# Performance work log

Measured on AMD Instinct MI355X. Metric: run time of the kernel, lower is better.

The kernel has to match this reference:

```python
import jax, jax.numpy as jnp
import numpy as np

B, CIN, H, W = 8, 64, 128, 128
COUT, K = 64, 3
STRIDE, PAD, DIL, G = 1, 1, 1, 1
T = K * K
HO = (H + 2 * PAD - (DIL * (K - 1) + 1)) // STRIDE + 1
WO = (W + 2 * PAD - (DIL * (K - 1) + 1)) // STRIDE + 1


def setup_inputs() -> dict:
    key = jax.random.key(0)
    ks = jax.random.split(key, 5)
    x = jax.random.normal(ks[0], (B, CIN, H, W), jnp.float32)
    offset = jax.random.normal(ks[1], (B, 2 * G * T, HO, WO), jnp.float32)
    mask = jax.random.uniform(ks[2], (B, G * T, HO, WO), jnp.float32)
    weight = jax.random.normal(ks[3], (COUT, CIN, K, K), jnp.float32) * (1.0 / np.sqrt(CIN * T))
    bias = jnp.zeros((COUT,), jnp.float32)
    return {"x": x, "offset": offset, "mask": mask, "weight": weight, "bias": bias}


def _gather(img_f, idx):
    # img_f: [Cg, H*W], idx: [T, Ho, Wo] -> [Cg, T, Ho, Wo]
    return img_f[:, idx]


def _dcn(x, offset, mask, weight, bias):
    Bn, Cin, Hh, Ww = x.shape
    Cout = weight.shape[0]
    Cg = Cin // G
    # offset channels laid out as [G, T, (dy, dx)] per DCNv2 convention
    off = offset.reshape(Bn, G, T, 2, HO, WO)
    dy, dx = off[:, :, :, 0], off[:, :, :, 1]  # [B, G, T, Ho, Wo]
    ky, kx = jnp.meshgrid(jnp.arange(K), jnp.arange(K), indexing="ij")
    ky = (ky.reshape(T) * DIL).astype(jnp.float32)
    kx = (kx.reshape(T) * DIL).astype(jnp.float32)
    base_y = (jnp.arange(HO) * STRIDE - PAD).astype(jnp.float32)
    base_x = (jnp.arange(WO) * STRIDE - PAD).astype(jnp.float32)
    # absolute sampling coordinates per (batch, def-group, tap, out-row, out-col)
    py = dy + base_y[None, None, None, :, None] + ky[None, None, :, None, None]
    px = dx + base_x[None, None, None, None, :] + kx[None, None, :, None, None]
    y0 = jnp.floor(py)
    x0 = jnp.floor(px)
    imgf = x.reshape(Bn, G, Cg, Hh * Ww)
    gather = jax.vmap(jax.vmap(_gather))  # over B and G
    sampled = jnp.zeros((Bn, G, Cg, T, HO, WO), x.dtype)
    # bilinear interpolation with zero padding outside the image
    for oy, ox in ((y0, x0), (y0, x0 + 1.0), (y0 + 1.0, x0), (y0 + 1.0, x0 + 1.0)):
        wgt = (1.0 - jnp.abs(py - oy)) * (1.0 - jnp.abs(px - ox))
        valid = (oy >= 0) & (oy < Hh) & (ox >= 0) & (ox < Ww)
        yi = jnp.clip(oy, 0, Hh - 1).astype(jnp.int32)
        xi = jnp.clip(ox, 0, Ww - 1).astype(jnp.int32)
        vals = gather(imgf, yi * Ww + xi)  # [B, G, Cg, T, Ho, Wo]
        sampled = sampled + vals * (wgt * valid)[:, :, None]
    # modulation mask, then accumulate taps into output channels
    m = mask.reshape(Bn, G, T, HO, WO)
    sampled = sampled * m[:, :, None]
    wr = weight.reshape(Cout, G, Cg, T)
    out = jnp.einsum("bgctij,ogct->boij", sampled, wr) + bias[None, :, None, None]
    return out


def reference(x, offset, mask, weight, bias):
    return _dcn(x, offset, mask, weight, bias)
```

## Files before the change

### kernel.cpp

```cpp
#include <hip/hip_runtime.h>
#include <stdint.h>

#define Bn   8
#define CIN  64
#define Hh   128
#define Wh   128
#define COUT 64
#define Tt   9
#define HO   128
#define WO   128
#define HW   (HO * WO)

#define RH     15
#define RWC    23
#define RREC   (RH * RWC)
#define RSTR   144
#define HALO_Y 3
#define HALO_X 3

typedef _Float16 h16;
typedef __attribute__((ext_vector_type(2)))  _Float16 h2;
typedef __attribute__((ext_vector_type(8)))  _Float16 h8;
typedef __attribute__((ext_vector_type(16))) float    f16v;

__device__ h16 g_xT[(size_t)Bn * Hh * Wh * CIN];
__device__ h16 g_wh[Tt * 4 * 2 * 64 * 8];

__global__ __launch_bounds__(256) void prep(const float* __restrict__ x,
                                            const float* __restrict__ w) {
    if (blockIdx.x >= Bn * Hh) {
        int tid = (blockIdx.x - Bn * Hh) * 256 + threadIdx.x;
        int t   = tid >> 12;
        int rem = tid & 4095;
        int ks  = rem >> 10;
        int mt  = (rem >> 9) & 1;
        int ln  = (rem >> 3) & 63;
        int j   = rem & 7;
        int o   = mt * 32 + (ln & 31);
        int c   = ks * 16 + ((ln >> 5) << 3) + j;
        g_wh[tid] = (h16)w[(size_t)(o * 64 + c) * 9 + t];
        return;
    }
    int b = blockIdx.x >> 7;
    int y = blockIdx.x & 127;
    __shared__ uint32_t tile[64][65];

    const float* src = x + ((size_t)b * CIN) * (Hh * Wh) + (size_t)y * Wh;
    int t    = threadIdx.x;
    int xp   = t & 63;
    int csub = t >> 6;
    #pragma unroll
    for (int cc = 0; cc < 64; cc += 4) {
        int c = cc + csub;
        float2 v = *(const float2*)(src + (size_t)c * (Hh * Wh) + xp * 2);
        uint32_t h0 = (uint32_t)__builtin_bit_cast(uint16_t, (h16)v.x);
        uint32_t h1 = (uint32_t)__builtin_bit_cast(uint16_t, (h16)v.y);
        tile[c][xp] = h0 | (h1 << 16);
    }
    __syncthreads();

    uint32_t* dst = (uint32_t*)(g_xT + (((size_t)b * Hh + y) * Wh) * CIN);
    int d  = t & 31;
    int xo = t >> 5;
    #pragma unroll
    for (int it = 0; it < 16; ++it) {
        int xg = it * 8 + xo;
        uint32_t lo = tile[2 * d][xg >> 1];
        uint32_t hi = tile[2 * d + 1][xg >> 1];
        int sh = (xg & 1) * 16;
        uint32_t l0 = (lo >> sh) & 0xffffu;
        uint32_t h1 = (hi >> sh) & 0xffffu;
        dst[xg * 32 + d] = l0 | (h1 << 16);
    }
}

__global__ __launch_bounds__(256, 3) void dcn_main(
        const float* __restrict__ offset, const float* __restrict__ mask,
        const float* __restrict__ bias, float* __restrict__ out) {
    __shared__ __align__(16) uint8_t sreg[RREC * RSTR];

    int blk  = blockIdx.x;
    int b    = blk & 7;
    int s    = blk >> 3;
    int ty   = s >> 3, tx = s & 7;
    int i0   = ty * 8, j0 = tx * 16;
    int lane = threadIdx.x & 63;
    int wave = threadIdx.x >> 6;
    int n    = lane & 31;
    int g    = lane >> 5;

    const h16* xb = g_xT + (size_t)b * (Hh * Wh * CIN);

    int i = i0 + 2 * wave + (n >> 4);
    int j = j0 + (n & 15);
    int p = (i << 7) + j;

    const float* offB = offset + (size_t)b * (2 * Tt * HW);
    const float* mskB = mask   + (size_t)b * (Tt * HW);
    float dyv[Tt], dxv[Tt], mmv[Tt];
    #pragma unroll
    for (int t = 0; t < Tt; ++t) {
        dyv[t] = offB[(2 * t) * HW + p];
        dxv[t] = offB[(2 * t + 1) * HW + p];
        mmv[t] = mskB[t * HW + p];
    }

    {
        const int base_y = i0 - HALO_Y, base_x = j0 - HALO_X;
        #pragma unroll
        for (int it = 0; it < 11; ++it) {
            int idx  = it * 256 + threadIdx.x;
            int rec  = idx >> 3;
            int quad = idx & 7;
            if (rec < RREC) {
                int ry = rec / RWC, rx = rec - ry * RWC;
                int gy = min(max(base_y + ry, 0), Hh - 1);
                int gx = min(max(base_x + rx, 0), Wh - 1);
                uint4 v = *(const uint4*)(xb + ((gy << 7) + gx) * 64 + quad * 8);
                *(uint4*)(sreg + rec * RSTR + quad * 16) = v;
            }
        }
    }
    __syncthreads();

    f16v acc[2] = {};

    #pragma unroll
    for (int t = 0; t < Tt; ++t) {
        const int ky = t / 3, kx = t % 3;
        float py = dyv[t] + (float)(i + ky - 1);
        float px = dxv[t] + (float)(j + kx - 1);
        float fy = floorf(py), fx = floorf(px);
        int   y0 = (int)fy,    x0 = (int)fx;
        float ly = py - fy,    lx = px - fx;
        float hy = 1.f - ly,   hx = 1.f - lx;

        bool vy0 = (y0 >= 0) && (y0 < Hh);
        bool vy1 = (y0 >= -1) && (y0 < Hh - 1);
        bool vx0 = (x0 >= 0) && (x0 < Wh);
        bool vx1 = (x0 >= -1) && (x0 < Wh - 1);
        float m = mmv[t];
        float w00 = (vy0 && vx0) ? hy * hx * m : 0.f;
        float w01 = (vy0 && vx1) ? hy * lx * m : 0.f;
        float w10 = (vy1 && vx0) ? ly * hx * m : 0.f;
        float w11 = (vy1 && vx1) ? ly * lx * m : 0.f;

        int ry = y0 - i0 + HALO_Y;
        int rx = x0 - j0 + HALO_X;
        bool intile = (ry >= 0) & (ry <= RH - 2) & (rx >= 0) & (rx <= RWC - 2);
        int ryc = min(max(ry, 0), RH - 2), rxc = min(max(rx, 0), RWC - 2);
        int pl00 = ryc * RWC + rxc;
        const uint8_t* cbase = sreg + pl00 * RSTR + g * 16;

        bool fb_any = __any(!intile);
        const h16 *f00 = nullptr, *f01 = nullptr, *f10 = nullptr, *f11 = nullptr;
        if (fb_any) {
            int y0c = min(max(y0, 0), Hh - 1), y1c = min(max(y0 + 1, 0), Hh - 1);
            int x0c = min(max(x0, 0), Wh - 1), x1c = min(max(x0 + 1, 0), Wh - 1);
            const h16* r0 = xb + (size_t)(y0c * Wh) * CIN;
            const h16* r1 = xb + (size_t)(y1c * Wh) * CIN;
            f00 = r0 + x0c * CIN + g * 8;
            f01 = r0 + x1c * CIN + g * 8;
            f10 = r1 + x0c * CIN + g * 8;
            f11 = r1 + x1c * CIN + g * 8;
        }

        h2 W00 = {(h16)w00, (h16)w00};
        h2 W01 = {(h16)w01, (h16)w01};
        h2 W10 = {(h16)w10, (h16)w10};
        h2 W11 = {(h16)w11, (h16)w11};

        const h16* wt = g_wh + t * 4096;
        union U4 { uint4 v; h2 h[4]; };
        #pragma unroll
        for (int ks = 0; ks < 4; ++ks) {
            U4 c00, c01, c10, c11;
            const uint8_t* cb = cbase + ks * 32;
            c00.v = *(const uint4*)(cb);
            c01.v = *(const uint4*)(cb + RSTR);
            c10.v = *(const uint4*)(cb + RWC * RSTR);
            c11.v = *(const uint4*)(cb + (RWC + 1) * RSTR);
            if (fb_any) {
                if (!intile) {
                    c00.v = *(const uint4*)(f00 + ks * 16);
                    c01.v = *(const uint4*)(f01 + ks * 16);
                    c10.v = *(const uint4*)(f10 + ks * 16);
                    c11.v = *(const uint4*)(f11 + ks * 16);
                }
            }
            union { h2 r[4]; h8 v; } pk;
            #pragma unroll
            for (int e = 0; e < 4; ++e) {
                h2 r = c00.h[e] * W00;
                r = c01.h[e] * W01 + r;
                r = c10.h[e] * W10 + r;
                r = c11.h[e] * W11 + r;
                pk.r[e] = r;
            }
            #pragma unroll
            for (int mt = 0; mt < 2; ++mt) {
                h8 a = *(const h8*)(wt + (ks * 2 + mt) * 512 + lane * 8);
                acc[mt] = __builtin_amdgcn_mfma_f32_32x32x16_f16(
                    a, pk.v, acc[mt], 0, 0, 0);
            }
        }
    }

    #pragma unroll
    for (int mt = 0; mt < 2; ++mt) {
        #pragma unroll
        for (int r = 0; r < 16; ++r) {
            int o = mt * 32 + (r & 3) + 8 * (r >> 2) + 4 * g;
            out[(size_t)(b * COUT + o) * HW + p] = acc[mt][r] + bias[o];
        }
    }
}

extern "C" void kernel_launch(void* const* d_in, const int* in_sizes, int n_in,
                              void* d_out, int out_size, void* d_ws, size_t ws_size,
                              hipStream_t stream) {
    const float* x      = (const float*)d_in[0];
    const float* offset = (const float*)d_in[1];
    const float* mask   = (const float*)d_in[2];
    const float* weight = (const float*)d_in[3];
    const float* bias   = (const float*)d_in[4];
    (void)d_ws; (void)ws_size;

    prep<<<Bn * Hh + 144, 256, 0, stream>>>(x, weight);
    dcn_main<<<Bn * 128, 256, 0, stream>>>(offset, mask, bias, (float*)d_out);
}
```

Baseline: 127.9 us.

## Drop LDS halo staging and gather bilinear corners directly from global memory

Removes the shared-memory staging of each block's 15x23 channel-last halo region, along with the fallback path for samples outside the tile. Every bilinear corner is now gathered directly from the global fp16 NHWC copy, relying on L1/L2 caching. Without LDS, occupancy rises and launch bounds go from 3 to 4 blocks per CU. The cost is more global/L2 gather traffic and latency, since nearby taps that previously hit LDS now go through the cache hierarchy.

```diff
diff --git a/kernel.cpp b/kernel.cpp
--- a/kernel.cpp
+++ b/kernel.cpp
@@ -10,13 +10,6 @@
 #define HO   128
 #define WO   128
 #define HW   (HO * WO)
-
-#define RH     15
-#define RWC    23
-#define RREC   (RH * RWC)
-#define RSTR   144
-#define HALO_Y 3
-#define HALO_X 3
 
 typedef _Float16 h16;
 typedef __attribute__((ext_vector_type(2)))  _Float16 h2;
@@ -74,11 +67,9 @@
     }
 }
 
-__global__ __launch_bounds__(256, 3) void dcn_main(
+__global__ __launch_bounds__(256, 4) void dcn_main(
         const float* __restrict__ offset, const float* __restrict__ mask,
         const float* __restrict__ bias, float* __restrict__ out) {
-    __shared__ __align__(16) uint8_t sreg[RREC * RSTR];
-
     int blk  = blockIdx.x;
     int b    = blk & 7;
     int s    = blk >> 3;
@@ -105,24 +96,6 @@
         mmv[t] = mskB[t * HW + p];
     }
 
-    {
-        const int base_y = i0 - HALO_Y, base_x = j0 - HALO_X;
-        #pragma unroll
-        for (int it = 0; it < 11; ++it) {
-            int idx  = it * 256 + threadIdx.x;
-            int rec  = idx >> 3;
-            int quad = idx & 7;
-            if (rec < RREC) {
-                int ry = rec / RWC, rx = rec - ry * RWC;
-                int gy = min(max(base_y + ry, 0), Hh - 1);
-                int gx = min(max(base_x + rx, 0), Wh - 1);
-                uint4 v = *(const uint4*)(xb + ((gy << 7) + gx) * 64 + quad * 8);
-                *(uint4*)(sreg + rec * RSTR + quad * 16) = v;
-            }
-        }
-    }
-    __syncthreads();
-
     f16v acc[2] = {};
 
     #pragma unroll
@@ -145,25 +118,12 @@
         float w10 = (vy1 && vx0) ? ly * hx * m : 0.f;
         float w11 = (vy1 && vx1) ? ly * lx * m : 0.f;
 
-        int ry = y0 - i0 + HALO_Y;
-        int rx = x0 - j0 + HALO_X;
-        bool intile = (ry >= 0) & (ry <= RH - 2) & (rx >= 0) & (rx <= RWC - 2);
-        int ryc = min(max(ry, 0), RH - 2), rxc = min(max(rx, 0), RWC - 2);
-        int pl00 = ryc * RWC + rxc;
-        const uint8_t* cbase = sreg + pl00 * RSTR + g * 16;
-
-        bool fb_any = __any(!intile);
-        const h16 *f00 = nullptr, *f01 = nullptr, *f10 = nullptr, *f11 = nullptr;
-        if (fb_any) {
-            int y0c = min(max(y0, 0), Hh - 1), y1c = min(max(y0 + 1, 0), Hh - 1);
-            int x0c = min(max(x0, 0), Wh - 1), x1c = min(max(x0 + 1, 0), Wh - 1);
-            const h16* r0 = xb + (size_t)(y0c * Wh) * CIN;
-            const h16* r1 = xb + (size_t)(y1c * Wh) * CIN;
-            f00 = r0 + x0c * CIN + g * 8;
-            f01 = r0 + x1c * CIN + g * 8;
-            f10 = r1 + x0c * CIN + g * 8;
-            f11 = r1 + x1c * CIN + g * 8;
-        }
+        int y0c = min(max(y0, 0), Hh - 1), y1c = min(max(y0 + 1, 0), Hh - 1);
+        int x0c = min(max(x0, 0), Wh - 1), x1c = min(max(x0 + 1, 0), Wh - 1);
+        const h16* p00 = xb + (((y0c << 7) | x0c) << 6) + g * 8;
+        const h16* p01 = xb + (((y0c << 7) | x1c) << 6) + g * 8;
+        const h16* p10 = xb + (((y1c << 7) | x0c) << 6) + g * 8;
+        const h16* p11 = xb + (((y1c << 7) | x1c) << 6) + g * 8;
 
         h2 W00 = {(h16)w00, (h16)w00};
         h2 W01 = {(h16)w01, (h16)w01};
@@ -175,19 +135,10 @@
         #pragma unroll
         for (int ks = 0; ks < 4; ++ks) {
             U4 c00, c01, c10, c11;
-            const uint8_t* cb = cbase + ks * 32;
-            c00.v = *(const uint4*)(cb);
-            c01.v = *(const uint4*)(cb + RSTR);
-            c10.v = *(const uint4*)(cb + RWC * RSTR);
-            c11.v = *(const uint4*)(cb + (RWC + 1) * RSTR);
-            if (fb_any) {
-                if (!intile) {
-                    c00.v = *(const uint4*)(f00 + ks * 16);
-                    c01.v = *(const uint4*)(f01 + ks * 16);
-                    c10.v = *(const uint4*)(f10 + ks * 16);
-                    c11.v = *(const uint4*)(f11 + ks * 16);
-                }
-            }
+            c00.v = *(const uint4*)(p00 + ks * 16);
+            c01.v = *(const uint4*)(p01 + ks * 16);
+            c10.v = *(const uint4*)(p10 + ks * 16);
+            c11.v = *(const uint4*)(p11 + ks * 16);
             union { h2 r[4]; h8 v; } pk;
             #pragma unroll
             for (int e = 0; e < 4; ++e) {
```

Result: slower. 173.1 us (+35.4%).
